# Kernel optimization log

Hardware: AMD Instinct MI355X
Metric: run time of the kernel (lower is better)

Reference implementation:

```python
import jax, jax.numpy as jnp
import numpy as np

N, DEG, F_IN, HID, OUT = 20000, 16, 128, 128, 64
E = N * DEG


def setup_inputs() -> dict:
    key = jax.random.key(0)
    ks = jax.random.split(key, 12)
    s = 0.05  # small init scale to keep activations stable
    x = jax.random.normal(ks[0], (N, F_IN), jnp.float32)
    # PyG LSTM aggregation requires edges sorted by destination; fixed degree DEG
    src = jax.random.randint(ks[1], (E,), 0, N, dtype=jnp.int32)
    dst = jnp.repeat(jnp.arange(N, dtype=jnp.int32), DEG)
    edge_index = jnp.stack([src, dst])  # [2, E]
    return {
        "x": x,
        "edge_index": edge_index,
        "lstm_Wih": jax.random.normal(ks[2], (4, 4 * HID, F_IN), jnp.float32) * s,
        "lstm_Whh": jax.random.normal(ks[3], (4, 4 * HID, HID), jnp.float32) * s,
        "lstm_bih": jax.random.normal(ks[4], (4, 4 * HID), jnp.float32) * s,
        "lstm_bhh": jax.random.normal(ks[5], (4, 4 * HID), jnp.float32) * s,
        "linl_W123": jax.random.normal(ks[6], (3, HID, HID), jnp.float32) * s,
        "linl_b123": jax.random.normal(ks[7], (3, HID), jnp.float32) * s,
        "linr_W123": jax.random.normal(ks[8], (3, HID, HID), jnp.float32) * s,
        "linl_W4": jax.random.normal(ks[9], (OUT, HID), jnp.float32) * s,
        "linl_b4": jax.random.normal(ks[10], (OUT,), jnp.float32) * s,
        "linr_W4": jax.random.normal(ks[11], (OUT, HID), jnp.float32) * s,
    }


def _lstm_last(msgs, Wih, Whh, bih, bhh):
    """Run an LSTM over the padded neighbor sequence, return h at last step.
    msgs: [n, deg, f]. Matches PyG LSTMAggregation (lstm(x)[0][:, -1])."""
    n = msgs.shape[0]
    H = Whh.shape[1]
    b = bih + bhh  # torch LSTM adds both biases

    def step(carry, xt):  # xt: [n, f]
        h, c = carry
        g = xt @ Wih.T + h @ Whh.T + b  # [n, 4H], gate order i,f,g,o
        i, f, gg, o = jnp.split(g, 4, axis=-1)
        c = jax.nn.sigmoid(f) * c + jax.nn.sigmoid(i) * jnp.tanh(gg)
        h = jax.nn.sigmoid(o) * jnp.tanh(c)
        return (h, c), None

    h0 = jnp.zeros((n, H), msgs.dtype)
    (h, _), _ = jax.lax.scan(step, (h0, h0), jnp.swapaxes(msgs, 0, 1))
    return h


def _sage_conv(x, src, Wih, Whh, bih, bhh, Wl, bl, Wr):
    """SAGEConv(aggr='lstm'): lin_l(lstm_agg(x_j)) + lin_r(x).
    Fixed degree + dst-sorted edges => to_dense_batch is a reshape."""
    n, f = x.shape
    msgs = x[src].reshape(n, DEG, f)  # gather neighbor (source) features
    agg = _lstm_last(msgs, Wih, Whh, bih, bhh)
    return agg @ Wl.T + bl + x @ Wr.T  # lin_r has no bias in PyG


def reference(x, edge_index, lstm_Wih, lstm_Whh, lstm_bih, lstm_bhh,
              linl_W123, linl_b123, linr_W123, linl_W4, linl_b4, linr_W4):
    src = edge_index[0]
    # eval mode: dropout is identity
    x1 = jax.nn.relu(_sage_conv(x, src, lstm_Wih[0], lstm_Whh[0], lstm_bih[0],
                                lstm_bhh[0], linl_W123[0], linl_b123[0], linr_W123[0]))
    x2 = jax.nn.relu(_sage_conv(x1, src, lstm_Wih[1], lstm_Whh[1], lstm_bih[1],
                                lstm_bhh[1], linl_W123[1], linl_b123[1], linr_W123[1]) + x1)
    x3 = jax.nn.relu(_sage_conv(x2, src, lstm_Wih[2], lstm_Whh[2], lstm_bih[2],
                                lstm_bhh[2], linl_W123[2], linl_b123[2], linr_W123[2]) + x2)
    x4 = _sage_conv(x3, src, lstm_Wih[3], lstm_Whh[3], lstm_bih[3], lstm_bhh[3],
                    linl_W4, linl_b4, linr_W4)
    return x4
```

## Files before the change

kernel.cpp:

```cpp
#include <hip/hip_runtime.h>


#define N_NODES 20000
#define DEG 16
#define NPB 80
#define RT 5

typedef __bf16 bf16x8 __attribute__((ext_vector_type(8)));
typedef float f32x4 __attribute__((ext_vector_type(4)));

__device__ inline unsigned short f2bf(float f) {
  unsigned u = __builtin_bit_cast(unsigned, f);
  u += 0x7fffu + ((u >> 16) & 1u);
  return (unsigned short)(u >> 16);
}
__device__ inline float fexp2(float x) {
#if __has_builtin(__builtin_amdgcn_exp2f)
  return __builtin_amdgcn_exp2f(x);
#else
  return exp2f(x);
#endif
}
__device__ inline float frcp(float x) {
#if __has_builtin(__builtin_amdgcn_rcpf)
  return __builtin_amdgcn_rcpf(x);
#else
  return 1.f / x;
#endif
}
__device__ inline float sigm(float x) { return frcp(1.f + fexp2(-1.44269504f * x)); }
__device__ inline float tanh_(float x) { return frcp(1.f + fexp2(-2.88539008f * x)) * 2.f - 1.f; }

__device__ inline void barrier_lds() {
  asm volatile("s_waitcnt lgkmcnt(0)\n\ts_barrier" ::: "memory");
}

__global__ __launch_bounds__(256) void prep_weights(
    const float* __restrict__ Wih, const float* __restrict__ Whh,
    const float* __restrict__ bih, const float* __restrict__ bhh,
    unsigned short* __restrict__ WihB, unsigned short* __restrict__ WhhB,
    float* __restrict__ bsum) {
  int tid = blockIdx.x * 256 + threadIdx.x;
  float4 a = *(const float4*)(Wih + tid * 4);
  ushort4 o;
  o.x = f2bf(a.x); o.y = f2bf(a.y); o.z = f2bf(a.z); o.w = f2bf(a.w);
  *(ushort4*)(WihB + tid * 4) = o;
  float4 b = *(const float4*)(Whh + tid * 4);
  ushort4 p;
  p.x = f2bf(b.x); p.y = f2bf(b.y); p.z = f2bf(b.z); p.w = f2bf(b.w);
  *(ushort4*)(WhhB + tid * 4) = p;
  if (tid < 2048) bsum[tid] = bih[tid] + bhh[tid];
}

__global__ __launch_bounds__(256) void cast_bf(
    const float* __restrict__ x, unsigned short* __restrict__ xb) {
  int tid = blockIdx.x * 256 + threadIdx.x;
  float4 v = *(const float4*)(x + tid * 4);
  ushort4 o;
  o.x = f2bf(v.x); o.y = f2bf(v.y); o.z = f2bf(v.z); o.w = f2bf(v.w);
  *(ushort4*)(xb + tid * 4) = o;
}

__global__ __launch_bounds__(512, 2) void lstm_fused(
    const unsigned short* __restrict__ xbf,
    const int* __restrict__ src,
    const unsigned short* __restrict__ WihB,
    const unsigned short* __restrict__ WhhB,
    const float* __restrict__ bsum,
    float* __restrict__ agg) {
  __shared__ __align__(16) unsigned char xsb[2][NPB * 256];
  __shared__ __align__(16) unsigned char hbuf[2][NPB * 256];
  __shared__ __align__(16) int idx_s[NPB * DEG];
  const int tid = threadIdx.x;
  const int lane = tid & 63, w = tid >> 6;
  const int l15 = lane & 15, l4 = lane >> 4;
  const int node0 = blockIdx.x * NPB;
  const int colb = w * 16 + l15;

#pragma unroll
  for (int i = 0; i < 3; ++i) {
    int task = tid + i * 512;
    if (task < NPB * DEG) {
      int node = task >> 4, t = task & 15;
      idx_s[t * NPB + node] = src[node0 * DEG + task];
    }
  }

  bf16x8 bwx[4][4], bwh[4][4];
  float bs[4];
#pragma unroll
  for (int g = 0; g < 4; ++g) {
#pragma unroll
    for (int kt = 0; kt < 4; ++kt) {
      bwx[g][kt] = *(const bf16x8*)(WihB + (g * 128 + colb) * 128 + kt * 32 + l4 * 8);
      bwh[g][kt] = *(const bf16x8*)(WhhB + (g * 128 + colb) * 128 + kt * 32 + l4 * 8);
    }
    bs[g] = bsum[g * 128 + colb];
  }
  barrier_lds();

  const int task0 = tid, task1 = tid + 512;
  const int row0s = task0 >> 4, ch0 = task0 & 15;
  const int row1s = task1 >> 4, ch1 = task1 & 15;
  const int task2 = tid + 1024;
  const bool p2 = task2 < NPB * 16;
  const int row2s = task2 >> 4, ch2 = task2 & 15;

  {
    uint4 v0 = *(const uint4*)(xbf + idx_s[row0s] * 128 + (ch0 ^ (row0s & 7)) * 8);
    uint4 v1 = *(const uint4*)(xbf + idx_s[row1s] * 128 + (ch1 ^ (row1s & 7)) * 8);
    *(uint4*)(&xsb[0][row0s * 256 + ch0 * 16]) = v0;
    *(uint4*)(&xsb[0][row1s * 256 + ch1 * 16]) = v1;
    if (p2) {
      uint4 v2 = *(const uint4*)(xbf + idx_s[row2s] * 128 + (ch2 ^ (row2s & 7)) * 8);
      *(uint4*)(&xsb[0][row2s * 256 + ch2 * 16]) = v2;
    }
  }
  barrier_lds();

  float c[RT][4];
#pragma unroll
  for (int rt = 0; rt < RT; ++rt)
#pragma unroll
    for (int r = 0; r < 4; ++r) c[rt][r] = 0.f;

#pragma unroll 2
  for (int t = 0; t < 16; ++t) {
    uint4 xstg0, xstg1, xstg2;
    if (t < 15) {
      const int tb = (t + 1) * NPB;
      xstg0 = *(const uint4*)(xbf + idx_s[tb + row0s] * 128 + (ch0 ^ (row0s & 7)) * 8);
      xstg1 = *(const uint4*)(xbf + idx_s[tb + row1s] * 128 + (ch1 ^ (row1s & 7)) * 8);
      if (p2)
        xstg2 = *(const uint4*)(xbf + idx_s[tb + row2s] * 128 + (ch2 ^ (row2s & 7)) * 8);
    }

    const unsigned char* xrb = xsb[t & 1];
    const unsigned char* hb = hbuf[(t + 1) & 1];
    unsigned char* hw = hbuf[t & 1];

#pragma unroll
    for (int rt = 0; rt < RT; ++rt) {
      f32x4 acc[4];
#pragma unroll
      for (int g = 0; g < 4; ++g) acc[g] = (f32x4){bs[g], bs[g], bs[g], bs[g]};

      const int m = rt * 16 + l15;
#pragma unroll
      for (int kt = 0; kt < 4; ++kt) {
        int byte = (m * 256 + kt * 64 + l4 * 16) ^ ((m & 7) << 4);
        bf16x8 a = *(const bf16x8*)(xrb + byte);
#pragma unroll
        for (int g = 0; g < 4; ++g)
          acc[g] = __builtin_amdgcn_mfma_f32_16x16x32_bf16(a, bwx[g][kt], acc[g], 0, 0, 0);
      }
      if (t > 0) {
#pragma unroll
        for (int kt = 0; kt < 4; ++kt) {
          int byte = (m * 256 + kt * 64 + l4 * 16) ^ ((m & 7) << 4);
          bf16x8 a = *(const bf16x8*)(hb + byte);
#pragma unroll
          for (int g = 0; g < 4; ++g)
            acc[g] = __builtin_amdgcn_mfma_f32_16x16x32_bf16(a, bwh[g][kt], acc[g], 0, 0, 0);
        }
      }

#pragma unroll
      for (int r = 0; r < 4; ++r) {
        float ig = sigm(acc[0][r]), fg = sigm(acc[1][r]);
        float gg = tanh_(acc[2][r]), og = sigm(acc[3][r]);
        float cn = fg * c[rt][r] + ig * gg;
        c[rt][r] = cn;
        float hv = og * tanh_(cn);
        int mm = rt * 16 + l4 * 4 + r;
        if (t < 15) {
          int byte = (mm * 256 + colb * 2) ^ ((mm & 7) << 4);
          *(__bf16*)(hw + byte) = (__bf16)hv;
        } else {
          agg[(node0 + mm) * 128 + colb] = hv;
        }
      }
    }

    if (t < 15) {
      unsigned char* xw = xsb[(t + 1) & 1];
      *(uint4*)(&xw[row0s * 256 + ch0 * 16]) = xstg0;
      *(uint4*)(&xw[row1s * 256 + ch1 * 16]) = xstg1;
      if (p2) *(uint4*)(&xw[row2s * 256 + ch2 * 16]) = xstg2;
      barrier_lds();
    }
  }
}

__global__ __launch_bounds__(256) void gemm_out(
    const float* __restrict__ A1,
    const float* __restrict__ A2,
    const float* __restrict__ Wl, const float* __restrict__ bl,
    const float* __restrict__ Wr,
    const float* __restrict__ resid,
    float* __restrict__ out,
    unsigned short* __restrict__ outbf,
    int NOUT, int do_relu, int Nrows) {
  __shared__ __align__(16) unsigned char As[64 * 512];
  const int tid = threadIdx.x;
  const int lane = tid & 63, w = tid >> 6;
  const int l15 = lane & 15, l4 = lane >> 4;
  const int row0 = blockIdx.x * 64;

#pragma unroll
  for (int i = 0; i < 16; ++i) {
    int flat = i * 1024 + tid * 4;
    int r = flat >> 8, c = flat & 255;
    int grow = row0 + r;
    float4 v;
    if (grow < Nrows)
      v = (c < 128) ? *(const float4*)(A1 + grow * 128 + c)
                    : *(const float4*)(A2 + grow * 128 + (c - 128));
    else
      v = make_float4(0.f, 0.f, 0.f, 0.f);
    ushort4 b;
    b.x = f2bf(v.x); b.y = f2bf(v.y); b.z = f2bf(v.z); b.w = f2bf(v.w);
    int byte = (r * 512 + c * 2) ^ ((r & 7) << 4);
    *(ushort4*)(As + byte) = b;
  }
  __syncthreads();

  const int colg = blockIdx.y * 64 + w * 16 + l15;
  bf16x8 bw[8];
#pragma unroll
  for (int kt = 0; kt < 8; ++kt) {
    const float* bp = (kt < 4) ? (Wl + colg * 128 + kt * 32 + l4 * 8)
                               : (Wr + colg * 128 + (kt - 4) * 32 + l4 * 8);
    float4 a = *(const float4*)bp;
    float4 b = *(const float4*)(bp + 4);
    bf16x8 v;
    v[0] = (__bf16)a.x; v[1] = (__bf16)a.y; v[2] = (__bf16)a.z; v[3] = (__bf16)a.w;
    v[4] = (__bf16)b.x; v[5] = (__bf16)b.y; v[6] = (__bf16)b.z; v[7] = (__bf16)b.w;
    bw[kt] = v;
  }

  f32x4 acc[4];
#pragma unroll
  for (int rt = 0; rt < 4; ++rt) acc[rt] = (f32x4){0.f, 0.f, 0.f, 0.f};

#pragma unroll
  for (int kt = 0; kt < 8; ++kt) {
#pragma unroll
    for (int rt = 0; rt < 4; ++rt) {
      int m = rt * 16 + l15;
      int byte = (m * 512 + kt * 64 + l4 * 16) ^ ((m & 7) << 4);
      bf16x8 af = *(const bf16x8*)(As + byte);
      acc[rt] = __builtin_amdgcn_mfma_f32_16x16x32_bf16(af, bw[kt], acc[rt], 0, 0, 0);
    }
  }

  const float bias = bl[colg];
#pragma unroll
  for (int rt = 0; rt < 4; ++rt)
#pragma unroll
    for (int r = 0; r < 4; ++r) {
      int grow = row0 + rt * 16 + l4 * 4 + r;
      if (grow < Nrows) {
        float v = acc[rt][r] + bias;
        if (resid) v += resid[grow * 128 + colg];
        if (do_relu) v = fmaxf(v, 0.f);
        out[grow * NOUT + colg] = v;
        if (outbf) outbf[grow * 128 + colg] = f2bf(v);
      }
    }
}

extern "C" void kernel_launch(void* const* d_in, const int* in_sizes, int n_in,
                              void* d_out, int out_size, void* d_ws, size_t ws_size,
                              hipStream_t stream) {
  const float* X = (const float*)d_in[0];
  const int* src = (const int*)d_in[1];
  const float* Wih = (const float*)d_in[2];
  const float* Whh = (const float*)d_in[3];
  const float* bih = (const float*)d_in[4];
  const float* bhh = (const float*)d_in[5];
  const float* Wl123 = (const float*)d_in[6];
  const float* bl123 = (const float*)d_in[7];
  const float* Wr123 = (const float*)d_in[8];
  const float* Wl4 = (const float*)d_in[9];
  const float* bl4 = (const float*)d_in[10];
  const float* Wr4 = (const float*)d_in[11];
  float* out = (float*)d_out;

  char* ws = (char*)d_ws;
  unsigned short* xbf = (unsigned short*)ws;
  float* agg = (float*)(ws + 5120000);
  float* xb0 = (float*)(ws + 15360000);
  float* xb1 = (float*)(ws + 25600000);
  unsigned short* WihB = (unsigned short*)(ws + 35840000);
  unsigned short* WhhB = (unsigned short*)(ws + 36364288);
  float* bsumW = (float*)(ws + 36888576);

  prep_weights<<<dim3(256), 256, 0, stream>>>(Wih, Whh, bih, bhh, WihB, WhhB, bsumW);
  cast_bf<<<dim3(2500), 256, 0, stream>>>(X, xbf);

  const float* xcur = X;
  for (int L = 0; L < 4; ++L) {
    lstm_fused<<<dim3(250), 512, 0, stream>>>(xbf, src, WihB + L * 65536,
                                              WhhB + L * 65536, bsumW + L * 512, agg);
    if (L < 3) {
      float* nxt = (L & 1) ? xb1 : xb0;
      gemm_out<<<dim3(313, 2), 256, 0, stream>>>(agg, xcur, Wl123 + L * 16384,
                                                 bl123 + L * 128, Wr123 + L * 16384,
                                                 (L >= 1) ? xcur : nullptr, nxt, xbf,
                                                 128, 1, N_NODES);
      xcur = nxt;
    } else {
      gemm_out<<<dim3(313, 1), 256, 0, stream>>>(agg, xcur, Wl4, bl4, Wr4, nullptr, out,
                                                 nullptr, 64, 0, N_NODES);
    }
  }
}
```

Measured before the change: 467.9 us.

## Load gathered neighbor features directly into MFMA registers, dropping LDS staging

Removes the shared-memory double buffer for gathered x rows. Each wave now loads its MFMA A-operand fragments straight from global memory, with a register double buffer prefetching the next row tile or timestep. The goal is to cut LDS traffic, the staging stores and the LDS footprint. In exchange, all 8 waves redundantly fetch the same rows from global or L2, which raises global load traffic, and register pressure grows.

```diff
diff --git a/kernel.cpp b/kernel.cpp
--- a/kernel.cpp
+++ b/kernel.cpp
@@ -68,7 +68,6 @@
     const unsigned short* __restrict__ WhhB,
     const float* __restrict__ bsum,
     float* __restrict__ agg) {
-  __shared__ __align__(16) unsigned char xsb[2][NPB * 256];
   __shared__ __align__(16) unsigned char hbuf[2][NPB * 256];
   __shared__ __align__(16) int idx_s[NPB * DEG];
   const int tid = threadIdx.x;
@@ -99,69 +98,62 @@
   }
   barrier_lds();
 
-  const int task0 = tid, task1 = tid + 512;
-  const int row0s = task0 >> 4, ch0 = task0 & 15;
-  const int row1s = task1 >> 4, ch1 = task1 & 15;
-  const int task2 = tid + 1024;
-  const bool p2 = task2 < NPB * 16;
-  const int row2s = task2 >> 4, ch2 = task2 & 15;
-
-  {
-    uint4 v0 = *(const uint4*)(xbf + idx_s[row0s] * 128 + (ch0 ^ (row0s & 7)) * 8);
-    uint4 v1 = *(const uint4*)(xbf + idx_s[row1s] * 128 + (ch1 ^ (row1s & 7)) * 8);
-    *(uint4*)(&xsb[0][row0s * 256 + ch0 * 16]) = v0;
-    *(uint4*)(&xsb[0][row1s * 256 + ch1 * 16]) = v1;
-    if (p2) {
-      uint4 v2 = *(const uint4*)(xbf + idx_s[row2s] * 128 + (ch2 ^ (row2s & 7)) * 8);
-      *(uint4*)(&xsb[0][row2s * 256 + ch2 * 16]) = v2;
-    }
-  }
-  barrier_lds();
-
   float c[RT][4];
 #pragma unroll
   for (int rt = 0; rt < RT; ++rt)
 #pragma unroll
     for (int r = 0; r < 4; ++r) c[rt][r] = 0.f;
+
+  bf16x8 xf[2][4];
+#define XISSUE(T2, RT2, B)                                            \
+  {                                                                   \
+    int row_ = idx_s[(T2) * NPB + (RT2) * 16 + l15];                  \
+    const unsigned short* rp_ = xbf + row_ * 128 + l4 * 8;            \
+    xf[B][0] = *(const bf16x8*)(rp_);                                 \
+    xf[B][1] = *(const bf16x8*)(rp_ + 32);                            \
+    xf[B][2] = *(const bf16x8*)(rp_ + 64);                            \
+    xf[B][3] = *(const bf16x8*)(rp_ + 96);                            \
+  }
+
+  XISSUE(0, 0, 0)
 
 #pragma unroll 2
   for (int t = 0; t < 16; ++t) {
-    uint4 xstg0, xstg1, xstg2;
-    if (t < 15) {
-      const int tb = (t + 1) * NPB;
-      xstg0 = *(const uint4*)(xbf + idx_s[tb + row0s] * 128 + (ch0 ^ (row0s & 7)) * 8);
-      xstg1 = *(const uint4*)(xbf + idx_s[tb + row1s] * 128 + (ch1 ^ (row1s & 7)) * 8);
-      if (p2)
-        xstg2 = *(const uint4*)(xbf + idx_s[tb + row2s] * 128 + (ch2 ^ (row2s & 7)) * 8);
-    }
-
-    const unsigned char* xrb = xsb[t & 1];
     const unsigned char* hb = hbuf[(t + 1) & 1];
     unsigned char* hw = hbuf[t & 1];
 
 #pragma unroll
-    for (int rt = 0; rt < RT; ++rt) {
+    for (int rti = 0; rti < RT; ++rti) {
+      const int cb = (t + rti) & 1;
+      const int ib = (t + rti + 1) & 1;
+
+      if (rti < RT - 1) {
+        XISSUE(t, rti + 1, ib)
+      } else if (t + 1 < 16) {
+        XISSUE(t + 1, 0, ib)
+      }
+
       f32x4 acc[4];
 #pragma unroll
       for (int g = 0; g < 4; ++g) acc[g] = (f32x4){bs[g], bs[g], bs[g], bs[g]};
 
-      const int m = rt * 16 + l15;
-#pragma unroll
-      for (int kt = 0; kt < 4; ++kt) {
-        int byte = (m * 256 + kt * 64 + l4 * 16) ^ ((m & 7) << 4);
-        bf16x8 a = *(const bf16x8*)(xrb + byte);
+#pragma unroll
+      for (int kt = 0; kt < 4; ++kt)
 #pragma unroll
         for (int g = 0; g < 4; ++g)
-          acc[g] = __builtin_amdgcn_mfma_f32_16x16x32_bf16(a, bwx[g][kt], acc[g], 0, 0, 0);
-      }
+          acc[g] = __builtin_amdgcn_mfma_f32_16x16x32_bf16(xf[cb][kt], bwx[g][kt],
+                                                           acc[g], 0, 0, 0);
+
       if (t > 0) {
+        const int m = rti * 16 + l15;
 #pragma unroll
         for (int kt = 0; kt < 4; ++kt) {
           int byte = (m * 256 + kt * 64 + l4 * 16) ^ ((m & 7) << 4);
           bf16x8 a = *(const bf16x8*)(hb + byte);
 #pragma unroll
           for (int g = 0; g < 4; ++g)
-            acc[g] = __builtin_amdgcn_mfma_f32_16x16x32_bf16(a, bwh[g][kt], acc[g], 0, 0, 0);
+            acc[g] = __builtin_amdgcn_mfma_f32_16x16x32_bf16(a, bwh[g][kt], acc[g],
+                                                             0, 0, 0);
         }
       }
 
@@ -169,10 +161,10 @@
       for (int r = 0; r < 4; ++r) {
         float ig = sigm(acc[0][r]), fg = sigm(acc[1][r]);
         float gg = tanh_(acc[2][r]), og = sigm(acc[3][r]);
-        float cn = fg * c[rt][r] + ig * gg;
-        c[rt][r] = cn;
+        float cn = fg * c[rti][r] + ig * gg;
+        c[rti][r] = cn;
         float hv = og * tanh_(cn);
-        int mm = rt * 16 + l4 * 4 + r;
+        int mm = rti * 16 + l4 * 4 + r;
         if (t < 15) {
           int byte = (mm * 256 + colb * 2) ^ ((mm & 7) << 4);
           *(__bf16*)(hw + byte) = (__bf16)hv;
@@ -182,14 +174,9 @@
       }
     }
 
-    if (t < 15) {
-      unsigned char* xw = xsb[(t + 1) & 1];
-      *(uint4*)(&xw[row0s * 256 + ch0 * 16]) = xstg0;
-      *(uint4*)(&xw[row1s * 256 + ch1 * 16]) = xstg1;
-      if (p2) *(uint4*)(&xw[row2s * 256 + ch2 * 16]) = xstg2;
-      barrier_lds();
-    }
-  }
+    if (t < 15) barrier_lds();
+  }
+#undef XISSUE
 }
 
 __global__ __launch_bounds__(256) void gemm_out(
```

Result: slower. 668.3 us (+42.8%).
